# Kernel tuning notes

Measured on AMD Instinct MI355X. Metric: run time of the kernel, lower is better.

## Reference

```python
import jax, jax.numpy as jnp
import numpy as np

# shapes
B, S, D, V = 2, 2048, 1024, 32000
C = 8            # n_cycles
P = 256          # actual planes = min(n_planes_init, D // 2)
EPS = 1.1920929e-07  # torch RMSNorm default eps for float32 (finfo.eps)


def _rmsnorm(x, w):
    ms = jnp.mean(x * x, axis=-1, keepdims=True)
    return x * jax.lax.rsqrt(ms + EPS) * w


def setup_inputs() -> dict:
    key = jax.random.key(0)
    ks = jax.random.split(key, 10)
    tokens = jax.random.randint(ks[0], (B, S), 0, V, dtype=jnp.int32)
    embed_weight = jax.random.normal(ks[1], (V, D), dtype=jnp.float32) * 0.02
    lm_head_weight = jax.random.normal(ks[2], (V, D), dtype=jnp.float32) * 0.02
    out_norm_weight = jnp.ones((D,), dtype=jnp.float32)
    # per-cycle learned params (non-trivial values for numerics)
    angles = jax.random.normal(ks[3], (C, P), dtype=jnp.float32) * 0.1
    scales = 1.0 + jax.random.normal(ks[4], (C, D), dtype=jnp.float32) * 0.01
    shifts = jax.random.normal(ks[5], (C, D), dtype=jnp.float32) * 0.01
    norm_weights = 1.0 + jax.random.normal(ks[6], (C, D), dtype=jnp.float32) * 0.01
    mix_weight = jnp.array([0.1, 0.8, 0.1], dtype=jnp.float32)
    # plane pairs: per-cycle permutation of D, pi = perm[:P], pj = perm[P:2P]
    pi_list, pj_list = [], []
    for c in range(C):
        perm = jax.random.permutation(jax.random.fold_in(ks[7], c), D)
        pi_list.append(perm[:P])
        pj_list.append(perm[P:2 * P])
    pi_all = jnp.stack(pi_list).astype(jnp.int32)  # [C, P]
    pj_all = jnp.stack(pj_list).astype(jnp.int32)  # [C, P]
    return {
        "tokens": tokens,
        "embed_weight": embed_weight,
        "angles": angles,
        "scales": scales,
        "shifts": shifts,
        "norm_weights": norm_weights,
        "mix_weight": mix_weight,
        "out_norm_weight": out_norm_weight,
        "lm_head_weight": lm_head_weight,
        "pi_all": pi_all,
        "pj_all": pj_all,
    }


def reference(tokens, embed_weight, angles, scales, shifts, norm_weights,
              mix_weight, out_norm_weight, lm_head_weight, pi_all, pj_all):
    x = embed_weight[tokens].astype(jnp.float32)  # [B, S, D]
    n_cycles = angles.shape[0]
    for c in range(n_cycles):
        # temporal mix: shifted-left / self / shifted-right
        left = jnp.pad(x[:, :-1, :], ((0, 0), (1, 0), (0, 0)))
        right = jnp.pad(x[:, 1:, :], ((0, 0), (0, 1), (0, 0)))
        x = mix_weight[0] * left + mix_weight[1] * x + mix_weight[2] * right
        # Givens rotations on disjoint plane pairs (gather -> rotate -> scatter)
        pi, pj = pi_all[c], pj_all[c]
        cos_a = jnp.cos(angles[c])
        sin_a = jnp.sin(angles[c])
        xi = x[..., pi]  # [B, S, P]
        xj = x[..., pj]
        x_new = x.at[..., pi].set(xi * cos_a - xj * sin_a)
        x_new = x_new.at[..., pj].set(xi * sin_a + xj * cos_a)
        # scale/shift + SiLU, then RMSNorm residual update
        x_act = jax.nn.silu(x_new * scales[c] + shifts[c])
        x = x + _rmsnorm(x_act - x, norm_weights[c])
    x = _rmsnorm(x, out_norm_weight)
    return jnp.einsum("bsd,vd->bsv", x, lm_head_weight)  # [B, S, V]
```

## Files before the change

### kernel.cpp

```cpp
#include <hip/hip_runtime.h>

#define B_SZ   2
#define S_LEN  2048
#define D_DIM  1024
#define V_DIM  32000
#define NTOK   (B_SZ * S_LEN)
#define NCYC   8
#define NPLANES 256
#define EPS_F  1.1920929e-07f

typedef float  f32x4  __attribute__((ext_vector_type(4)));
typedef __bf16 bf16x8 __attribute__((ext_vector_type(8)));

__device__ __forceinline__ unsigned short f32_to_bf16(float f) {
    unsigned int u = __builtin_bit_cast(unsigned int, f);
    u += 0x7fffu + ((u >> 16) & 1u);
    return (unsigned short)(u >> 16);
}

__device__ __forceinline__ float4 mix3(float a, const float4& u, float b,
                                       const float4& v, float c, const float4& w) {
    return make_float4(a * u.x + b * v.x + c * w.x,
                       a * u.y + b * v.y + c * w.y,
                       a * u.z + b * v.z + c * w.z,
                       a * u.w + b * v.w + c * w.w);
}

__global__ __launch_bounds__(256) void k_cyc(
    int c,
    const int* __restrict__ tokens, const float* __restrict__ table,
    const float* __restrict__ xin, float* __restrict__ xout,
    const float* __restrict__ angles, const float* __restrict__ scales,
    const float* __restrict__ shifts, const float* __restrict__ normw,
    const float* __restrict__ mixw, const float* __restrict__ outnw,
    unsigned short* __restrict__ xbf,
    const int* __restrict__ pi, const int* __restrict__ pj,
    const float* __restrict__ lmhead, unsigned short* __restrict__ wbf)
{
    __shared__ float lx[4][D_DIM];
    __shared__ float red[4][4];
    const int b = blockIdx.x, tid = threadIdx.x;
    const int wv = tid >> 6, ln = tid & 63;
    const int t0 = b << 2;
    const int s0 = t0 & (S_LEN - 1);

    float4 row[4];
    float4 hl = make_float4(0.f, 0.f, 0.f, 0.f);
    float4 hr = make_float4(0.f, 0.f, 0.f, 0.f);
    if (c == 0) {
        #pragma unroll
        for (int i = 0; i < 4; ++i) {
            const int tok = tokens[t0 + i];
            row[i] = ((const float4*)(table + (size_t)tok * D_DIM))[tid];
        }
        if (s0 > 0) {
            const int tok = tokens[t0 - 1];
            hl = ((const float4*)(table + (size_t)tok * D_DIM))[tid];
        }
        if (s0 + 4 < S_LEN) {
            const int tok = tokens[t0 + 4];
            hr = ((const float4*)(table + (size_t)tok * D_DIM))[tid];
        }
    } else {
        #pragma unroll
        for (int i = 0; i < 4; ++i)
            row[i] = ((const float4*)(xin + (size_t)(t0 + i) * D_DIM))[tid];
        if (s0 > 0)
            hl = ((const float4*)(xin + (size_t)(t0 - 1) * D_DIM))[tid];
        if (s0 + 4 < S_LEN)
            hr = ((const float4*)(xin + (size_t)(t0 + 4) * D_DIM))[tid];
    }
    const float mw0 = mixw[0], mw1 = mixw[1], mw2 = mixw[2];

    float4 m[4];
    m[0] = mix3(mw0, hl,     mw1, row[0], mw2, row[1]);
    m[1] = mix3(mw0, row[0], mw1, row[1], mw2, row[2]);
    m[2] = mix3(mw0, row[1], mw1, row[2], mw2, row[3]);
    m[3] = mix3(mw0, row[2], mw1, row[3], mw2, hr);
    #pragma unroll
    for (int i = 0; i < 4; ++i) ((float4*)lx[i])[tid] = m[i];
    __syncthreads();

    const int ip = pi[tid], jp = pj[tid];
    float sa, ca;
    sincosf(angles[tid], &sa, &ca);
    float xi[4], xj[4];
    #pragma unroll
    for (int i = 0; i < 4; ++i) { xi[i] = lx[i][ip]; xj[i] = lx[i][jp]; }
    #pragma unroll
    for (int i = 0; i < 4; ++i) {
        lx[i][ip] = xi[i] * ca - xj[i] * sa;
        lx[i][jp] = xi[i] * sa + xj[i] * ca;
    }
    __syncthreads();

    const float4 sc = ((const float4*)scales)[tid];
    const float4 sh = ((const float4*)shifts)[tid];
    const float4 nw = ((const float4*)normw)[tid];
    float4 r[4];
    float sum[4];
    #pragma unroll
    for (int i = 0; i < 4; ++i) {
        const float4 xn = ((const float4*)lx[i])[tid];
        const float a0 = xn.x * sc.x + sh.x;
        const float a1 = xn.y * sc.y + sh.y;
        const float a2 = xn.z * sc.z + sh.z;
        const float a3 = xn.w * sc.w + sh.w;
        r[i].x = a0 / (1.f + expf(-a0)) - m[i].x;
        r[i].y = a1 / (1.f + expf(-a1)) - m[i].y;
        r[i].z = a2 / (1.f + expf(-a2)) - m[i].z;
        r[i].w = a3 / (1.f + expf(-a3)) - m[i].w;
        sum[i] = r[i].x * r[i].x + r[i].y * r[i].y
               + r[i].z * r[i].z + r[i].w * r[i].w;
    }
    #pragma unroll
    for (int off = 32; off > 0; off >>= 1)
        #pragma unroll
        for (int i = 0; i < 4; ++i) sum[i] += __shfl_down(sum[i], off, 64);
    if (ln == 0) {
        red[wv][0] = sum[0]; red[wv][1] = sum[1];
        red[wv][2] = sum[2]; red[wv][3] = sum[3];
    }
    __syncthreads();
    #pragma unroll
    for (int i = 0; i < 4; ++i) {
        const float tot = red[0][i] + red[1][i] + red[2][i] + red[3][i];
        const float inv = rsqrtf(tot * (1.0f / D_DIM) + EPS_F);
        row[i].x = m[i].x + r[i].x * inv * nw.x;
        row[i].y = m[i].y + r[i].y * inv * nw.y;
        row[i].z = m[i].z + r[i].z * inv * nw.z;
        row[i].w = m[i].w + r[i].w * inv * nw.w;
    }

    if (c == 7) {
        __syncthreads();
        float fs[4];
        #pragma unroll
        for (int i = 0; i < 4; ++i)
            fs[i] = row[i].x * row[i].x + row[i].y * row[i].y
                  + row[i].z * row[i].z + row[i].w * row[i].w;
        #pragma unroll
        for (int off = 32; off > 0; off >>= 1)
            #pragma unroll
            for (int i = 0; i < 4; ++i) fs[i] += __shfl_down(fs[i], off, 64);
        if (ln == 0) {
            red[wv][0] = fs[0]; red[wv][1] = fs[1];
            red[wv][2] = fs[2]; red[wv][3] = fs[3];
        }
        __syncthreads();
        const float4 w = ((const float4*)outnw)[tid];
        #pragma unroll
        for (int i = 0; i < 4; ++i) {
            const float tot = red[0][i] + red[1][i] + red[2][i] + red[3][i];
            const float inv = rsqrtf(tot * (1.0f / D_DIM) + EPS_F);
            const ushort4 o = make_ushort4(f32_to_bf16(row[i].x * inv * w.x),
                                           f32_to_bf16(row[i].y * inv * w.y),
                                           f32_to_bf16(row[i].z * inv * w.z),
                                           f32_to_bf16(row[i].w * inv * w.w));
            ((ushort4*)xbf)[(size_t)(t0 + i) * 256 + tid] = o;
        }
    } else {
        #pragma unroll
        for (int i = 0; i < 4; ++i)
            ((float4*)(xout + (size_t)(t0 + i) * D_DIM))[tid] = row[i];
    }

    {
        const int end = (c + 1) * 1024000;
        for (int i = c * 1024000 + b * 256 + tid; i < end; i += 262144) {
            const float4 v = ((const float4*)lmhead)[i];
            const ushort4 o = make_ushort4(f32_to_bf16(v.x), f32_to_bf16(v.y),
                                           f32_to_bf16(v.z), f32_to_bf16(v.w));
            ((ushort4*)wbf)[i] = o;
        }
    }
}

#define GLD_LDS(g, l)                                                          \
    __builtin_amdgcn_global_load_lds(                                          \
        (const __attribute__((address_space(1))) void*)(g),                    \
        (__attribute__((address_space(3))) void*)(l), 16, 0, 0)

#define STAGE_A(BUF, H, KT) do {                                               \
    GLD_LDS(gA + (size_t)(H) * 131072 + (size_t)(KT) * 64,                     \
            &lds[(BUF) * 32768 + (H) * 8192 + wave * 1024]);                   \
    GLD_LDS(gA + (size_t)(H) * 131072 + 8192 + (size_t)(KT) * 64,              \
            &lds[(BUF) * 32768 + (H) * 8192 + wave * 1024 + 512]);             \
} while (0)

#define STAGE_B(BUF, H, KT) do {                                               \
    GLD_LDS(gB + (size_t)(H) * 131072 + (size_t)(KT) * 64,                     \
            &lds[16384 + (BUF) * 32768 + (H) * 8192 + wave * 1024]);           \
    GLD_LDS(gB + (size_t)(H) * 131072 + 8192 + (size_t)(KT) * 64,              \
            &lds[16384 + (BUF) * 32768 + (H) * 8192 + wave * 1024 + 512]);     \
} while (0)

#define RD_A(BUF, MIB) do { _Pragma("unroll")                                  \
    for (int q_ = 0; q_ < 4; ++q_) {                                           \
        afr[q_][0] = *(const bf16x8*)&lds[(BUF) * 32768 + aoff + ((MIB) + q_) * 1024 + kx0]; \
        afr[q_][1] = *(const bf16x8*)&lds[(BUF) * 32768 + aoff + ((MIB) + q_) * 1024 + kx1]; \
    } } while (0)

#define RD_B(BUF, NIB, DST) do { _Pragma("unroll")                             \
    for (int n_ = 0; n_ < 2; ++n_) {                                           \
        DST[n_][0] = *(const bf16x8*)&lds[(BUF) * 32768 + boff + ((NIB) + n_) * 1024 + kx0]; \
        DST[n_][1] = *(const bf16x8*)&lds[(BUF) * 32768 + boff + ((NIB) + n_) * 1024 + kx1]; \
    } } while (0)

#define MFMA16(MIB, NIB, BF) do {                                              \
    __builtin_amdgcn_s_setprio(1);                                             \
    _Pragma("unroll") for (int m_ = 0; m_ < 4; ++m_)                           \
    _Pragma("unroll") for (int n_ = 0; n_ < 2; ++n_) {                         \
        acc[(MIB) + m_][(NIB) + n_] = __builtin_amdgcn_mfma_f32_16x16x32_bf16( \
            afr[m_][0], BF[n_][0], acc[(MIB) + m_][(NIB) + n_], 0, 0, 0);      \
        acc[(MIB) + m_][(NIB) + n_] = __builtin_amdgcn_mfma_f32_16x16x32_bf16( \
            afr[m_][1], BF[n_][1], acc[(MIB) + m_][(NIB) + n_], 0, 0, 0);      \
    }                                                                          \
    __builtin_amdgcn_s_setprio(0); } while (0)

#define PH_SYNC() do { __builtin_amdgcn_s_barrier();                           \
    asm volatile("s_waitcnt lgkmcnt(0)" ::: "memory"); } while (0)
#define PH_END() do { asm volatile("" ::: "memory");                           \
    __builtin_amdgcn_s_barrier(); } while (0)
#define VMCNT4() asm volatile("s_waitcnt vmcnt(4)" ::: "memory")

__global__ __launch_bounds__(512, 2) void k_gemm(
    const unsigned short* __restrict__ A,
    const unsigned short* __restrict__ Bw,
    float* __restrict__ C)
{
    __shared__ __align__(16) unsigned short lds[65536];
    const int tid = threadIdx.x;
    const int wave = tid >> 6, lane = tid & 63;
    const int wm = wave >> 2, wn = wave & 3;
    const int lr = lane & 15, kg = lane >> 4;

    const int swz = (blockIdx.x & 7) * 250 + (blockIdx.x >> 3);
    const int bm = swz & 15, bn = swz >> 4;

    const int xr  = (lane & 7) * 8;
    const int kx0 = (kg * 8) ^ xr;
    const int kx1 = (32 + kg * 8) ^ xr;
    const int aoff = (wm * 128 + lr) * 64;
    const int boff = 16384 + (wn * 64 + lr) * 64;

    const int srow = lane >> 3;
    const int scol = ((lane & 7) ^ srow) * 8;
    const unsigned short* gA = A  + (size_t)(bm * 256 + wave * 16 + srow) * 1024 + scol;
    const unsigned short* gB = Bw + (size_t)(bn * 256 + wave * 16 + srow) * 1024 + scol;

    f32x4 acc[8][4];
    #pragma unroll
    for (int i = 0; i < 8; ++i)
        #pragma unroll
        for (int j = 0; j < 4; ++j) acc[i][j] = (f32x4){0.f, 0.f, 0.f, 0.f};
    bf16x8 afr[4][2], b01[2][2], b23[2][2];

    STAGE_A(0, 0, 0); STAGE_A(0, 1, 0);
    STAGE_B(0, 0, 0); STAGE_B(0, 1, 0);
    STAGE_B(1, 0, 1); STAGE_B(1, 1, 1);
    VMCNT4();
    __builtin_amdgcn_s_barrier();

    for (int j = 0; j < 8; ++j) {
        const int k1 = (2 * j + 1) & 15;
        const int k2 = (2 * j + 2) & 15;
        const int k3 = (2 * j + 3) & 15;

        RD_A(0, 0); RD_B(0, 0, b01);
        STAGE_A(1, 0, k1);
        PH_SYNC(); MFMA16(0, 0, b01); PH_END();

        RD_B(0, 2, b23);
        STAGE_A(1, 1, k1);
        PH_SYNC(); MFMA16(0, 2, b23); PH_END();

        RD_A(0, 4);
        STAGE_B(0, 0, k2);
        PH_SYNC(); MFMA16(4, 2, b23); PH_END();

        STAGE_B(0, 1, k2);
        VMCNT4();
        PH_SYNC(); MFMA16(4, 0, b01); PH_END();

        RD_A(1, 0); RD_B(1, 0, b01);
        STAGE_A(0, 0, k2);
        PH_SYNC(); MFMA16(0, 0, b01); PH_END();

        RD_B(1, 2, b23);
        STAGE_A(0, 1, k2);
        PH_SYNC(); MFMA16(0, 2, b23); PH_END();

        RD_A(1, 4);
        STAGE_B(1, 0, k3);
        PH_SYNC(); MFMA16(4, 2, b23); PH_END();

        STAGE_B(1, 1, k3);
        VMCNT4();
        PH_SYNC(); MFMA16(4, 0, b01); PH_END();
    }

    #pragma unroll
    for (int mi = 0; mi < 8; ++mi) {
        const size_t m0 = (size_t)(bm * 256 + wm * 128 + mi * 16 + kg * 4);
        #pragma unroll
        for (int ni = 0; ni < 4; ++ni) {
            const int n = bn * 256 + wn * 64 + ni * 16 + lr;
            float* cp = C + m0 * V_DIM + n;
            __builtin_nontemporal_store(acc[mi][ni][0], cp);
            __builtin_nontemporal_store(acc[mi][ni][1], cp + (size_t)V_DIM);
            __builtin_nontemporal_store(acc[mi][ni][2], cp + (size_t)2 * V_DIM);
            __builtin_nontemporal_store(acc[mi][ni][3], cp + (size_t)3 * V_DIM);
        }
    }
}

extern "C" void kernel_launch(void* const* d_in, const int* in_sizes, int n_in,
                              void* d_out, int out_size, void* d_ws, size_t ws_size,
                              hipStream_t stream)
{
    const int*   tokens = (const int*)  d_in[0];
    const float* embedw = (const float*)d_in[1];
    const float* angles = (const float*)d_in[2];
    const float* scales = (const float*)d_in[3];
    const float* shifts = (const float*)d_in[4];
    const float* normw  = (const float*)d_in[5];
    const float* mixw   = (const float*)d_in[6];
    const float* outnw  = (const float*)d_in[7];
    const float* lmhead = (const float*)d_in[8];
    const int*   pi_all = (const int*)  d_in[9];
    const int*   pj_all = (const int*)  d_in[10];
    float* out = (float*)d_out;

    float* xa = (float*)d_ws;
    float* xb = xa + (size_t)NTOK * D_DIM;
    unsigned short* xbf = (unsigned short*)(xb + (size_t)NTOK * D_DIM);
    unsigned short* wbf = xbf + (size_t)NTOK * D_DIM;

    for (int c = 0; c < NCYC; ++c) {
        const float* xin = (c & 1) ? xb : xa;
        float* xout = (c & 1) ? xa : xb;
        k_cyc<<<NTOK / 4, 256, 0, stream>>>(c, tokens, embedw, xin, xout,
            angles + c * NPLANES, scales + c * D_DIM, shifts + c * D_DIM,
            normw + c * D_DIM, mixw, outnw, xbf,
            pi_all + c * NPLANES, pj_all + c * NPLANES, lmhead, wbf);
    }

    k_gemm<<<16 * 125, 512, 0, stream>>>(xbf, wbf, out);
}
```

Before: 425.8 us.

## Make GEMM persistent with cross-tile prefetch of the next tile's operands

The GEMM becomes a persistent kernel with 256 blocks that walk the 2000 output tiles in strides of 256. During the last k-iteration each block prefetches the first k-slices of its next tile, so the pipeline stays full across tile boundaries and the prologue stall is paid once per block instead of once per tile. The block-index swizzle is dropped in favour of plain row-major tile order. The output stores become ordinary stores instead of nontemporal ones. This can cause wave-quantization imbalance (2000 tiles over 256 blocks), can hurt L2 reuse without the swizzle, and the new store path changes cache behaviour.

```diff
diff --git a/kernel.cpp b/kernel.cpp
--- a/kernel.cpp
+++ b/kernel.cpp
@@ -8,6 +8,7 @@
 #define NCYC   8
 #define NPLANES 256
 #define EPS_F  1.1920929e-07f
+#define NTILE  2000
 
 typedef float  f32x4  __attribute__((ext_vector_type(4)));
 typedef __bf16 bf16x8 __attribute__((ext_vector_type(8)));
@@ -181,17 +182,17 @@
         (const __attribute__((address_space(1))) void*)(g),                    \
         (__attribute__((address_space(3))) void*)(l), 16, 0, 0)
 
-#define STAGE_A(BUF, H, KT) do {                                               \
-    GLD_LDS(gA + (size_t)(H) * 131072 + (size_t)(KT) * 64,                     \
+#define STAGE_A(BUF, H, KT, P) do {                                            \
+    GLD_LDS((P) + (size_t)(H) * 131072 + (size_t)(KT) * 64,                    \
             &lds[(BUF) * 32768 + (H) * 8192 + wave * 1024]);                   \
-    GLD_LDS(gA + (size_t)(H) * 131072 + 8192 + (size_t)(KT) * 64,              \
+    GLD_LDS((P) + (size_t)(H) * 131072 + 8192 + (size_t)(KT) * 64,             \
             &lds[(BUF) * 32768 + (H) * 8192 + wave * 1024 + 512]);             \
 } while (0)
 
-#define STAGE_B(BUF, H, KT) do {                                               \
-    GLD_LDS(gB + (size_t)(H) * 131072 + (size_t)(KT) * 64,                     \
+#define STAGE_B(BUF, H, KT, P) do {                                            \
+    GLD_LDS((P) + (size_t)(H) * 131072 + (size_t)(KT) * 64,                    \
             &lds[16384 + (BUF) * 32768 + (H) * 8192 + wave * 1024]);           \
-    GLD_LDS(gB + (size_t)(H) * 131072 + 8192 + (size_t)(KT) * 64,              \
+    GLD_LDS((P) + (size_t)(H) * 131072 + 8192 + (size_t)(KT) * 64,             \
             &lds[16384 + (BUF) * 32768 + (H) * 8192 + wave * 1024 + 512]);     \
 } while (0)
 
@@ -235,9 +236,6 @@
     const int wm = wave >> 2, wn = wave & 3;
     const int lr = lane & 15, kg = lane >> 4;
 
-    const int swz = (blockIdx.x & 7) * 250 + (blockIdx.x >> 3);
-    const int bm = swz & 15, bn = swz >> 4;
-
     const int xr  = (lane & 7) * 8;
     const int kx0 = (kg * 8) ^ xr;
     const int kx1 = (32 + kg * 8) ^ xr;
@@ -246,72 +244,91 @@
 
     const int srow = lane >> 3;
     const int scol = ((lane & 7) ^ srow) * 8;
-    const unsigned short* gA = A  + (size_t)(bm * 256 + wave * 16 + srow) * 1024 + scol;
-    const unsigned short* gB = Bw + (size_t)(bn * 256 + wave * 16 + srow) * 1024 + scol;
-
-    f32x4 acc[8][4];
-    #pragma unroll
-    for (int i = 0; i < 8; ++i)
-        #pragma unroll
-        for (int j = 0; j < 4; ++j) acc[i][j] = (f32x4){0.f, 0.f, 0.f, 0.f};
+    const int soff = (wave * 16 + srow) * 1024 + scol;
+
+    int g  = blockIdx.x;
+    int bm = g & 15, bn = g >> 4;
+    const unsigned short* gA = A  + (size_t)(bm * 256) * 1024 + soff;
+    const unsigned short* gB = Bw + (size_t)(bn * 256) * 1024 + soff;
+
     bf16x8 afr[4][2], b01[2][2], b23[2][2];
 
-    STAGE_A(0, 0, 0); STAGE_A(0, 1, 0);
-    STAGE_B(0, 0, 0); STAGE_B(0, 1, 0);
-    STAGE_B(1, 0, 1); STAGE_B(1, 1, 1);
+    STAGE_A(0, 0, 0, gA); STAGE_A(0, 1, 0, gA);
+    STAGE_B(0, 0, 0, gB); STAGE_B(0, 1, 0, gB);
+    STAGE_B(1, 0, 1, gB); STAGE_B(1, 1, 1, gB);
     VMCNT4();
     __builtin_amdgcn_s_barrier();
 
-    for (int j = 0; j < 8; ++j) {
-        const int k1 = (2 * j + 1) & 15;
-        const int k2 = (2 * j + 2) & 15;
-        const int k3 = (2 * j + 3) & 15;
-
-        RD_A(0, 0); RD_B(0, 0, b01);
-        STAGE_A(1, 0, k1);
-        PH_SYNC(); MFMA16(0, 0, b01); PH_END();
-
-        RD_B(0, 2, b23);
-        STAGE_A(1, 1, k1);
-        PH_SYNC(); MFMA16(0, 2, b23); PH_END();
-
-        RD_A(0, 4);
-        STAGE_B(0, 0, k2);
-        PH_SYNC(); MFMA16(4, 2, b23); PH_END();
-
-        STAGE_B(0, 1, k2);
-        VMCNT4();
-        PH_SYNC(); MFMA16(4, 0, b01); PH_END();
-
-        RD_A(1, 0); RD_B(1, 0, b01);
-        STAGE_A(0, 0, k2);
-        PH_SYNC(); MFMA16(0, 0, b01); PH_END();
-
-        RD_B(1, 2, b23);
-        STAGE_A(0, 1, k2);
-        PH_SYNC(); MFMA16(0, 2, b23); PH_END();
-
-        RD_A(1, 4);
-        STAGE_B(1, 0, k3);
-        PH_SYNC(); MFMA16(4, 2, b23); PH_END();
-
-        STAGE_B(1, 1, k3);
-        VMCNT4();
-        PH_SYNC(); MFMA16(4, 0, b01); PH_END();
-    }
-
-    #pragma unroll
-    for (int mi = 0; mi < 8; ++mi) {
-        const size_t m0 = (size_t)(bm * 256 + wm * 128 + mi * 16 + kg * 4);
-        #pragma unroll
-        for (int ni = 0; ni < 4; ++ni) {
-            const int n = bn * 256 + wn * 64 + ni * 16 + lr;
-            float* cp = C + m0 * V_DIM + n;
-            __builtin_nontemporal_store(acc[mi][ni][0], cp);
-            __builtin_nontemporal_store(acc[mi][ni][1], cp + (size_t)V_DIM);
-            __builtin_nontemporal_store(acc[mi][ni][2], cp + (size_t)2 * V_DIM);
-            __builtin_nontemporal_store(acc[mi][ni][3], cp + (size_t)3 * V_DIM);
-        }
+    while (true) {
+        const int gn_raw = g + 256;
+        const bool last = (gn_raw >= NTILE);
+        const int gn = last ? g : gn_raw;
+        const int bm2 = gn & 15, bn2 = gn >> 4;
+        const unsigned short* gA2 = A  + (size_t)(bm2 * 256) * 1024 + soff;
+        const unsigned short* gB2 = Bw + (size_t)(bn2 * 256) * 1024 + soff;
+
+        f32x4 acc[8][4];
+        #pragma unroll
+        for (int i = 0; i < 8; ++i)
+            #pragma unroll
+            for (int j2 = 0; j2 < 4; ++j2) acc[i][j2] = (f32x4){0.f, 0.f, 0.f, 0.f};
+
+        for (int j = 0; j < 8; ++j) {
+            const unsigned short* sA = (j == 7) ? gA2 : gA;
+            const unsigned short* sB = (j == 7) ? gB2 : gB;
+            const int k1 = 2 * j + 1;
+            const int k2 = (2 * j + 2) & 15;
+            const int k3 = (2 * j + 3) & 15;
+
+            RD_A(0, 0); RD_B(0, 0, b01);
+            STAGE_A(1, 0, k1, gA);
+            PH_SYNC(); MFMA16(0, 0, b01); PH_END();
+
+            RD_B(0, 2, b23);
+            STAGE_A(1, 1, k1, gA);
+            PH_SYNC(); MFMA16(0, 2, b23); PH_END();
+
+            RD_A(0, 4);
+            STAGE_B(0, 0, k2, sB);
+            PH_SYNC(); MFMA16(4, 2, b23); PH_END();
+
+            STAGE_B(0, 1, k2, sB);
+            VMCNT4();
+            PH_SYNC(); MFMA16(4, 0, b01); PH_END();
+
+            RD_A(1, 0); RD_B(1, 0, b01);
+            STAGE_A(0, 0, k2, sA);
+            PH_SYNC(); MFMA16(0, 0, b01); PH_END();
+
+            RD_B(1, 2, b23);
+            STAGE_A(0, 1, k2, sA);
+            PH_SYNC(); MFMA16(0, 2, b23); PH_END();
+
+            RD_A(1, 4);
+            STAGE_B(1, 0, k3, sB);
+            PH_SYNC(); MFMA16(4, 2, b23); PH_END();
+
+            STAGE_B(1, 1, k3, sB);
+            VMCNT4();
+            PH_SYNC(); MFMA16(4, 0, b01); PH_END();
+        }
+
+        #pragma unroll
+        for (int mi = 0; mi < 8; ++mi) {
+            const size_t m0 = (size_t)(bm * 256 + wm * 128 + mi * 16 + kg * 4);
+            #pragma unroll
+            for (int ni = 0; ni < 4; ++ni) {
+                const int n = bn * 256 + wn * 64 + ni * 16 + lr;
+                float* cp = C + m0 * V_DIM + n;
+                cp[0]                 = acc[mi][ni][0];
+                cp[(size_t)V_DIM]     = acc[mi][ni][1];
+                cp[(size_t)2 * V_DIM] = acc[mi][ni][2];
+                cp[(size_t)3 * V_DIM] = acc[mi][ni][3];
+            }
+        }
+
+        if (last) break;
+        g = gn; bm = bm2; bn = bn2; gA = gA2; gB = gB2;
     }
 }
 
@@ -346,5 +363,5 @@
             pi_all + c * NPLANES, pj_all + c * NPLANES, lmhead, wbf);
     }
 
-    k_gemm<<<16 * 125, 512, 0, stream>>>(xbf, wbf, out);
-}
+    k_gemm<<<256, 512, 0, stream>>>(xbf, wbf, out);
+}
```

New measurement: 422.2 us. About the same (-0.8%).

## Replace 256x256 phased GEMM with simpler 128x128 double-buffered tile kernel

Applied to the files above, without the earlier changes.

Swaps the 512-thread, 256x256-tile GEMM with its eight-phase interleaved LDS staging schedule for a 256-thread, 128x128-tile kernel. The new kernel uses a plain double buffer: each k-step prefetches the next slice while running 32 MFMAs, with one barrier per step. Output stores become regular stores instead of nontemporal ones. This trades operand reuse per tile and the fine-grained overlap for lower register and LDS pressure and a simpler schedule, at the cost of more global traffic and more blocks.

```diff
diff --git a/kernel.cpp b/kernel.cpp
--- a/kernel.cpp
+++ b/kernel.cpp
@@ -181,138 +181,95 @@
         (const __attribute__((address_space(1))) void*)(g),                    \
         (__attribute__((address_space(3))) void*)(l), 16, 0, 0)
 
-#define STAGE_A(BUF, H, KT) do {                                               \
-    GLD_LDS(gA + (size_t)(H) * 131072 + (size_t)(KT) * 64,                     \
-            &lds[(BUF) * 32768 + (H) * 8192 + wave * 1024]);                   \
-    GLD_LDS(gA + (size_t)(H) * 131072 + 8192 + (size_t)(KT) * 64,              \
-            &lds[(BUF) * 32768 + (H) * 8192 + wave * 1024 + 512]);             \
-} while (0)
-
-#define STAGE_B(BUF, H, KT) do {                                               \
-    GLD_LDS(gB + (size_t)(H) * 131072 + (size_t)(KT) * 64,                     \
-            &lds[16384 + (BUF) * 32768 + (H) * 8192 + wave * 1024]);           \
-    GLD_LDS(gB + (size_t)(H) * 131072 + 8192 + (size_t)(KT) * 64,              \
-            &lds[16384 + (BUF) * 32768 + (H) * 8192 + wave * 1024 + 512]);     \
-} while (0)
-
-#define RD_A(BUF, MIB) do { _Pragma("unroll")                                  \
-    for (int q_ = 0; q_ < 4; ++q_) {                                           \
-        afr[q_][0] = *(const bf16x8*)&lds[(BUF) * 32768 + aoff + ((MIB) + q_) * 1024 + kx0]; \
-        afr[q_][1] = *(const bf16x8*)&lds[(BUF) * 32768 + aoff + ((MIB) + q_) * 1024 + kx1]; \
-    } } while (0)
-
-#define RD_B(BUF, NIB, DST) do { _Pragma("unroll")                             \
-    for (int n_ = 0; n_ < 2; ++n_) {                                           \
-        DST[n_][0] = *(const bf16x8*)&lds[(BUF) * 32768 + boff + ((NIB) + n_) * 1024 + kx0]; \
-        DST[n_][1] = *(const bf16x8*)&lds[(BUF) * 32768 + boff + ((NIB) + n_) * 1024 + kx1]; \
-    } } while (0)
-
-#define MFMA16(MIB, NIB, BF) do {                                              \
-    __builtin_amdgcn_s_setprio(1);                                             \
-    _Pragma("unroll") for (int m_ = 0; m_ < 4; ++m_)                           \
-    _Pragma("unroll") for (int n_ = 0; n_ < 2; ++n_) {                         \
-        acc[(MIB) + m_][(NIB) + n_] = __builtin_amdgcn_mfma_f32_16x16x32_bf16( \
-            afr[m_][0], BF[n_][0], acc[(MIB) + m_][(NIB) + n_], 0, 0, 0);      \
-        acc[(MIB) + m_][(NIB) + n_] = __builtin_amdgcn_mfma_f32_16x16x32_bf16( \
-            afr[m_][1], BF[n_][1], acc[(MIB) + m_][(NIB) + n_], 0, 0, 0);      \
-    }                                                                          \
-    __builtin_amdgcn_s_setprio(0); } while (0)
-
-#define PH_SYNC() do { __builtin_amdgcn_s_barrier();                           \
-    asm volatile("s_waitcnt lgkmcnt(0)" ::: "memory"); } while (0)
-#define PH_END() do { asm volatile("" ::: "memory");                           \
-    __builtin_amdgcn_s_barrier(); } while (0)
-#define VMCNT4() asm volatile("s_waitcnt vmcnt(4)" ::: "memory")
-
-__global__ __launch_bounds__(512, 2) void k_gemm(
+__global__ __launch_bounds__(256, 2) void k_gemm(
     const unsigned short* __restrict__ A,
     const unsigned short* __restrict__ Bw,
     float* __restrict__ C)
 {
-    __shared__ __align__(16) unsigned short lds[65536];
+    __shared__ __align__(16) unsigned short lds[2][16384];
     const int tid = threadIdx.x;
     const int wave = tid >> 6, lane = tid & 63;
-    const int wm = wave >> 2, wn = wave & 3;
+    const int wm = wave >> 1, wn = wave & 1;
     const int lr = lane & 15, kg = lane >> 4;
 
-    const int swz = (blockIdx.x & 7) * 250 + (blockIdx.x >> 3);
-    const int bm = swz & 15, bn = swz >> 4;
-
-    const int xr  = (lane & 7) * 8;
-    const int kx0 = (kg * 8) ^ xr;
-    const int kx1 = (32 + kg * 8) ^ xr;
-    const int aoff = (wm * 128 + lr) * 64;
-    const int boff = 16384 + (wn * 64 + lr) * 64;
+    const int x  = blockIdx.x & 7;
+    const int lb = blockIdx.x >> 3;
+    const int T  = x * 1000 + lb;
+    const int bm = T & 31, bn = T >> 5;
 
     const int srow = lane >> 3;
-    const int scol = ((lane & 7) ^ srow) * 8;
-    const unsigned short* gA = A  + (size_t)(bm * 256 + wave * 16 + srow) * 1024 + scol;
-    const unsigned short* gB = Bw + (size_t)(bn * 256 + wave * 16 + srow) * 1024 + scol;
-
-    f32x4 acc[8][4];
-    #pragma unroll
-    for (int i = 0; i < 8; ++i)
+    const int scg  = lane & 7;
+    const int scol = (scg ^ srow) * 8;
+    const unsigned short* gA = A  + (size_t)(bm * 128 + wave * 8 + srow) * 1024 + scol;
+    const unsigned short* gB = Bw + (size_t)(bn * 128 + wave * 8 + srow) * 1024 + scol;
+
+    const int sx = lane & 7;
+    const int ka = ((kg ^ sx) * 8);
+    const int kb = (((kg + 4) ^ sx) * 8);
+    const int arow = wm * 64 + lr;
+    const int brow = wn * 64 + lr;
+
+    f32x4 acc[4][4];
+    #pragma unroll
+    for (int i = 0; i < 4; ++i)
         #pragma unroll
         for (int j = 0; j < 4; ++j) acc[i][j] = (f32x4){0.f, 0.f, 0.f, 0.f};
-    bf16x8 afr[4][2], b01[2][2], b23[2][2];
-
-    STAGE_A(0, 0, 0); STAGE_A(0, 1, 0);
-    STAGE_B(0, 0, 0); STAGE_B(0, 1, 0);
-    STAGE_B(1, 0, 1); STAGE_B(1, 1, 1);
-    VMCNT4();
-    __builtin_amdgcn_s_barrier();
-
-    for (int j = 0; j < 8; ++j) {
-        const int k1 = (2 * j + 1) & 15;
-        const int k2 = (2 * j + 2) & 15;
-        const int k3 = (2 * j + 3) & 15;
-
-        RD_A(0, 0); RD_B(0, 0, b01);
-        STAGE_A(1, 0, k1);
-        PH_SYNC(); MFMA16(0, 0, b01); PH_END();
-
-        RD_B(0, 2, b23);
-        STAGE_A(1, 1, k1);
-        PH_SYNC(); MFMA16(0, 2, b23); PH_END();
-
-        RD_A(0, 4);
-        STAGE_B(0, 0, k2);
-        PH_SYNC(); MFMA16(4, 2, b23); PH_END();
-
-        STAGE_B(0, 1, k2);
-        VMCNT4();
-        PH_SYNC(); MFMA16(4, 0, b01); PH_END();
-
-        RD_A(1, 0); RD_B(1, 0, b01);
-        STAGE_A(0, 0, k2);
-        PH_SYNC(); MFMA16(0, 0, b01); PH_END();
-
-        RD_B(1, 2, b23);
-        STAGE_A(0, 1, k2);
-        PH_SYNC(); MFMA16(0, 2, b23); PH_END();
-
-        RD_A(1, 4);
-        STAGE_B(1, 0, k3);
-        PH_SYNC(); MFMA16(4, 2, b23); PH_END();
-
-        STAGE_B(1, 1, k3);
-        VMCNT4();
-        PH_SYNC(); MFMA16(4, 0, b01); PH_END();
-    }
-
-    #pragma unroll
-    for (int mi = 0; mi < 8; ++mi) {
-        const size_t m0 = (size_t)(bm * 256 + wm * 128 + mi * 16 + kg * 4);
+    bf16x8 af0[4], af1[4], bf0[4], bf1[4];
+
+#define STAGE(BUF, KT) do { _Pragma("unroll")                                  \
+    for (int r_ = 0; r_ < 4; ++r_) {                                           \
+        GLD_LDS(gA + (size_t)r_ * 32 * 1024 + (size_t)(KT) * 64,               \
+                &lds[BUF][r_ * 2048 + wave * 512]);                            \
+        GLD_LDS(gB + (size_t)r_ * 32 * 1024 + (size_t)(KT) * 64,               \
+                &lds[BUF][8192 + r_ * 2048 + wave * 512]);                     \
+    } } while (0)
+
+#define RDF(BUF) do { _Pragma("unroll")                                        \
+    for (int q_ = 0; q_ < 4; ++q_) {                                           \
+        af0[q_] = *(const bf16x8*)&lds[BUF][(arow + q_ * 16) * 64 + ka];       \
+        af1[q_] = *(const bf16x8*)&lds[BUF][(arow + q_ * 16) * 64 + kb];       \
+        bf0[q_] = *(const bf16x8*)&lds[BUF][8192 + (brow + q_ * 16) * 64 + ka];\
+        bf1[q_] = *(const bf16x8*)&lds[BUF][8192 + (brow + q_ * 16) * 64 + kb];\
+    } } while (0)
+
+    STAGE(0, 0);
+    __syncthreads();
+
+    int cur = 0;
+    for (int kt = 0; kt < 16; ++kt) {
+        const int ktn = (kt < 15) ? kt + 1 : 15;
+        STAGE(cur ^ 1, ktn);
+        RDF(cur);
+        __builtin_amdgcn_s_setprio(1);
+        #pragma unroll
+        for (int mi = 0; mi < 4; ++mi)
+            #pragma unroll
+            for (int ni = 0; ni < 4; ++ni) {
+                acc[mi][ni] = __builtin_amdgcn_mfma_f32_16x16x32_bf16(
+                    af0[mi], bf0[ni], acc[mi][ni], 0, 0, 0);
+                acc[mi][ni] = __builtin_amdgcn_mfma_f32_16x16x32_bf16(
+                    af1[mi], bf1[ni], acc[mi][ni], 0, 0, 0);
+            }
+        __builtin_amdgcn_s_setprio(0);
+        __syncthreads();
+        cur ^= 1;
+    }
+
+    #pragma unroll
+    for (int mi = 0; mi < 4; ++mi) {
+        const size_t m0 = (size_t)(bm * 128 + wm * 64 + mi * 16 + kg * 4);
         #pragma unroll
         for (int ni = 0; ni < 4; ++ni) {
-            const int n = bn * 256 + wn * 64 + ni * 16 + lr;
+            const int n = bn * 128 + wn * 64 + ni * 16 + lr;
             float* cp = C + m0 * V_DIM + n;
-            __builtin_nontemporal_store(acc[mi][ni][0], cp);
-            __builtin_nontemporal_store(acc[mi][ni][1], cp + (size_t)V_DIM);
-            __builtin_nontemporal_store(acc[mi][ni][2], cp + (size_t)2 * V_DIM);
-            __builtin_nontemporal_store(acc[mi][ni][3], cp + (size_t)3 * V_DIM);
-        }
-    }
+            cp[0]                 = acc[mi][ni][0];
+            cp[(size_t)V_DIM]     = acc[mi][ni][1];
+            cp[(size_t)2 * V_DIM] = acc[mi][ni][2];
+            cp[(size_t)3 * V_DIM] = acc[mi][ni][3];
+        }
+    }
+#undef STAGE
+#undef RDF
 }
 
 extern "C" void kernel_launch(void* const* d_in, const int* in_sizes, int n_in,
@@ -346,5 +303,5 @@
             pi_all + c * NPLANES, pj_all + c * NPLANES, lmhead, wbf);
     }
 
-    k_gemm<<<16 * 125, 512, 0, stream>>>(xbf, wbf, out);
-}
+    k_gemm<<<8000, 256, 0, stream>>>(xbf, wbf, out);
+}
```

After: 538.3 us. 1.26x slower.
